# Kernel tuning notes

Hardware: AMD Instinct MI355X
Metric: run time of the kernel (lower is better)

## Reference

```python
import jax, jax.numpy as jnp
import numpy as np
import math

D_MODEL = 1024
NUM_HEADS = 16
SEQ = 2048
BATCH = 4


def setup_inputs() -> dict:
    key = jax.random.key(0)
    ks = jax.random.split(key, 7)
    s = 0.02
    return {
        "x": jax.random.normal(ks[0], (BATCH, SEQ, D_MODEL), jnp.float32),
        "Wq": jax.random.normal(ks[1], (D_MODEL, D_MODEL), jnp.float32) * s,
        "bq": jax.random.normal(ks[2], (D_MODEL,), jnp.float32) * s,
        "Wkv": jax.random.normal(ks[3], (D_MODEL, 2 * D_MODEL), jnp.float32) * s,
        "bkv": jax.random.normal(ks[4], (2 * D_MODEL,), jnp.float32) * s,
        "Wo": jax.random.normal(ks[5], (D_MODEL, D_MODEL), jnp.float32) * s,
        "bo": jax.random.normal(ks[6], (D_MODEL,), jnp.float32) * s,
        "decoderMask": 1,
    }


def reference(x, Wq, bq, Wkv, bkv, Wo, bo, decoderMask):
    B, S, D = x.shape
    H = NUM_HEADS
    dh = D // H
    q_ = x @ Wq + bq              # [B,S,D]
    kv_ = x @ Wkv + bkv           # [B,S,2D] (self-attention: m is None)
    # Faithful to source: concat [q_, kv_] then reshape into heads of 3*dh,
    # which interleaves Q/KV projection columns across heads.
    qkv = jnp.concatenate([q_, kv_], axis=-1)          # [B,S,3D]
    qkv = qkv.reshape(B, S, H, 3 * dh).transpose(0, 2, 1, 3)  # [B,H,S,3dh]
    q, k, v = jnp.split(qkv, 3, axis=-1)               # each [B,H,S,dh]
    scaled = jnp.einsum("bhqd,bhkd->bhqk", q, k) / math.sqrt(dh)
    if decoderMask:
        mask = jnp.triu(jnp.full((S, S), -jnp.inf, dtype=scaled.dtype), k=1)
        scaled = scaled + mask
    attn = jax.nn.softmax(scaled, axis=-1)
    vals = jnp.einsum("bhqk,bhkd->bhqd", attn, v)      # [B,H,S,dh]
    vals = vals.transpose(0, 2, 1, 3).reshape(B, S, D)
    return vals @ Wo + bo
```

## Files before the change

### kernel.cpp

```cpp
#include <hip/hip_runtime.h>
#include <cstddef>
#include <cstdint>

#define SEQ   2048
#define BATCH 4
#define DM    1024
#define NH    16
#define DH    64
#define ROWS  (BATCH*SEQ)
#define NC3   3072
#define SM_SCALE 0.18033688f

typedef unsigned short u16;
typedef __attribute__((ext_vector_type(8))) short bf16x8;
typedef __attribute__((ext_vector_type(2))) float f32x2;
typedef __attribute__((ext_vector_type(4))) float f32x4;
typedef __attribute__((ext_vector_type(16))) float f32x16;
typedef __attribute__((ext_vector_type(4))) unsigned u32x4;
typedef __attribute__((ext_vector_type(2))) unsigned u32x2;

union V16 { f32x16 v; f32x2 p[8]; };

__device__ __forceinline__ u16 f2b(float f) {
  union { float f; unsigned u; } v; v.f = f;
  unsigned r = v.u + 0x7fffu + ((v.u >> 16) & 1u);
  return (u16)(r >> 16);
}

__device__ __forceinline__ unsigned cvt_pk_bf16(float lo, float hi) {
  unsigned r;
  asm("v_cvt_pk_bf16_f32 %0, %1, %2" : "=v"(r) : "v"(lo), "v"(hi));
  return r;
}

__device__ __forceinline__ void plswap(unsigned& a, unsigned& b) {
  auto rr = __builtin_amdgcn_permlane32_swap((int)a, (int)b, false, false);
  a = (unsigned)rr[0];
  b = (unsigned)rr[1];
}

__device__ __forceinline__ float ex2(float x) { return __builtin_amdgcn_exp2f(x); }

__device__ __forceinline__ void gld16(const void* g, void* l) {
  __builtin_amdgcn_global_load_lds((const __attribute__((address_space(1))) void*)g,
                                   (__attribute__((address_space(3))) void*)l,
                                   16, 0, 0);
}

__global__ __launch_bounds__(256) void prep_tw_kernel(
    const float* __restrict__ x, const float* __restrict__ bq,
    const float* __restrict__ bkv, u16* __restrict__ xb, float* __restrict__ bc,
    const float* __restrict__ Wq, const float* __restrict__ Wkv,
    const float* __restrict__ Wo, u16* __restrict__ Wt)
{
  __shared__ float t_[32][33];
  const int tid = threadIdx.x;
  if (blockIdx.x < 8192) {
    int i = blockIdx.x * 256 + tid;
    int idx = i * 4;
    float4 v = *(const float4*)(x + idx);
    xb[idx + 0] = f2b(v.x);
    xb[idx + 1] = f2b(v.y);
    xb[idx + 2] = f2b(v.z);
    xb[idx + 3] = f2b(v.w);
    if (i < NC3) bc[i] = (i < DM) ? bq[i] : bkv[i - DM];
  } else {
    const int bid = blockIdx.x - 8192;
    const int n0 = (bid & 127) * 32, k0 = (bid >> 7) * 32;
    const int xcol = tid & 31, yrow = tid >> 5;
    #pragma unroll
    for (int it = 0; it < 4; ++it) {
      int k = k0 + yrow + it * 8;
      int n = n0 + xcol;
      float v;
      if (n < DM)           v = Wq[k * DM + n];
      else if (n < NC3)     v = Wkv[k * (2 * DM) + (n - DM)];
      else                  v = Wo[k * DM + (n - NC3)];
      t_[yrow + it * 8][xcol] = v;
    }
    __syncthreads();
    #pragma unroll
    for (int it = 0; it < 4; ++it) {
      int n = n0 + yrow + it * 8;
      int k = k0 + xcol;
      Wt[(size_t)n * DM + k] = f2b(t_[xcol][yrow + it * 8]);
    }
  }
}

template <int MODE>
__global__ __launch_bounds__(256) void gemm_bt(
    const u16* __restrict__ A, const u16* __restrict__ Bt,
    const float* __restrict__ bias, void* __restrict__ C,
    u16* __restrict__ Vt, int M, int N, int K)
{
  __shared__ alignas(16) u16 lds_[3 * 8192];
  const int tid = threadIdx.x;
  const int lane = tid & 63, wid = tid >> 6;
  const int wr = (wid >> 1) * 64, wc = (wid & 1) * 64;
  const int l15 = lane & 15, lhi = lane >> 4;

  const int bid = blockIdx.x;
  const int xcd = bid & 7, t = bid >> 3;
  const int rsub = t & 7, colb = t >> 3;
  const int row0 = (xcd * 8 + rsub) * 128, col0 = colb * 128;
  const int sr = tid >> 2;
  const int scol = (((tid & 3) ^ ((sr >> 1) & 3)) * 8);

  const u16* aS0 = A  + (size_t)(row0 + sr) * K + scol;
  const u16* aS1 = A  + (size_t)(row0 + 64 + sr) * K + scol;
  const u16* bS0 = Bt + (size_t)(col0 + sr) * K + scol;
  const u16* bS1 = Bt + (size_t)(col0 + 64 + sr) * K + scol;
  const int dA = tid * 8;

  const int csw = ((lhi ^ ((l15 >> 1) & 3)) * 8);
  int aoff[4], boff[4];
  #pragma unroll
  for (int m = 0; m < 4; ++m) aoff[m] = (wr + m * 16 + l15) * 32 + csw;
  #pragma unroll
  for (int n = 0; n < 4; ++n) boff[n] = 4096 + (wc + n * 16 + l15) * 32 + csw;

  f32x4 acc[4][4];
  #pragma unroll
  for (int m = 0; m < 4; ++m)
    #pragma unroll
    for (int n = 0; n < 4; ++n) { f32x4 z = {0.f, 0.f, 0.f, 0.f}; acc[m][n] = z; }

  const int KT = K >> 5;

  auto stage = [&](int kt, u16* base) {
    const int ka = kt * 32;
    gld16(aS0 + ka, base + dA);
    gld16(aS1 + ka, base + 2048 + dA);
    gld16(bS0 + ka, base + 4096 + dA);
    gld16(bS1 + ka, base + 6144 + dA);
  };

  u16* const bufA = lds_;
  u16* const bufB = lds_ + 8192;
  u16* const bufC = lds_ + 16384;

  stage(0, bufA); stage(1, bufB);
  asm volatile("s_waitcnt vmcnt(4)" ::: "memory");
  __builtin_amdgcn_s_barrier();

  u16* rb = bufA;
  u16* sb = bufC;
  for (int kt = 0; kt < KT; ++kt) {
    bf16x8 a[4], b[4];
    #pragma unroll
    for (int m = 0; m < 4; ++m) a[m] = *(const bf16x8*)&rb[aoff[m]];
    #pragma unroll
    for (int n = 0; n < 4; ++n) b[n] = *(const bf16x8*)&rb[boff[n]];
    if (kt + 2 < KT) stage(kt + 2, sb);
    __builtin_amdgcn_s_setprio(1);
    #pragma unroll
    for (int m = 0; m < 4; ++m)
      #pragma unroll
      for (int n = 0; n < 4; ++n)
        acc[m][n] = __builtin_amdgcn_mfma_f32_16x16x32_bf16(a[m], b[n], acc[m][n], 0, 0, 0);
    __builtin_amdgcn_s_setprio(0);
    if (kt + 1 < KT) {
      if (kt + 2 < KT) { asm volatile("s_waitcnt vmcnt(4)" ::: "memory"); }
      else             { asm volatile("s_waitcnt vmcnt(0)" ::: "memory"); }
      __builtin_amdgcn_s_barrier();
    }
    rb = (rb == bufC) ? bufA : rb + 8192;
    sb = (sb == bufC) ? bufA : sb + 8192;
  }

  #pragma unroll
  for (int m = 0; m < 4; ++m)
    #pragma unroll
    for (int n = 0; n < 4; ++n) {
      const int col = col0 + wc + n * 16 + l15;
      const float bv = bias[col];
      if (MODE == 0) {
        #pragma unroll
        for (int r = 0; r < 4; ++r) {
          const int row = row0 + wr + m * 16 + lhi * 4 + r;
          ((float*)C)[(size_t)row * N + col] = acc[m][n][r] + bv;
        }
      } else {
        const int hh = col / 192;
        const int cc = col - hh * 192;
        if (cc < 128) {
          const float qs = (cc < 64) ? SM_SCALE : 1.f;
          #pragma unroll
          for (int r = 0; r < 4; ++r) {
            const int row = row0 + wr + m * 16 + lhi * 4 + r;
            ((u16*)C)[(size_t)row * N + col] = f2b((acc[m][n][r] + bv) * qs);
          }
        } else {
          u16 wv[4];
          #pragma unroll
          for (int r = 0; r < 4; ++r) wv[r] = f2b(acc[m][n][r] + bv);
          const int row = row0 + wr + m * 16 + lhi * 4;
          const int bb = row >> 11, j = row & (SEQ - 1);
          u16* vt = Vt + ((size_t)(bb * NH + hh) * 64 + (cc - 128)) * SEQ + j;
          u32x2 pv = { (unsigned)wv[0] | ((unsigned)wv[1] << 16),
                       (unsigned)wv[2] | ((unsigned)wv[3] << 16) };
          *(u32x2*)vt = pv;
        }
      }
    }
}

__global__ __launch_bounds__(256) void attn_kernel(
    const u16* __restrict__ qkv, const u16* __restrict__ Vt, u16* __restrict__ ctx)
{
  const int bid = blockIdx.x;
  const int p   = (bid >> 3) & 7;
  const int g   = (bid & 7) + ((bid >> 6) << 3);
  const int h   = g & 15, b = g >> 4;
  const int tid = threadIdx.x;
  const int lane = tid & 63, wid = tid >> 6;
  const int l31 = lane & 31, lhi5 = lane >> 5;

  __shared__ alignas(16) u16 smem[4 * 64 * 64];

  const size_t kv_row = (size_t)(b * NH + h) * 64;
  const int sr = tid >> 3, sck = tid & 7;
  const int scks = sck ^ (sr & 7);

  const u16* kSrc0 = qkv + (size_t)(b * SEQ + sr) * NC3 + h * 192 + 64 + scks * 8;
  const u16* kSrc1 = kSrc0 + (size_t)32 * NC3;
  const u16* vSrc0 = Vt + (kv_row + sr) * SEQ + scks * 8;
  const u16* vSrc1 = vSrc0 + (size_t)32 * SEQ;
  const int dOff0 = sr * 64 + sck * 8;
  const int dOff1 = (32 + sr) * 64 + sck * 8;

  int koff[4], koff2[4];
  #pragma unroll
  for (int c = 0; c < 4; ++c) {
    koff[c]  = l31 * 64        + (((2 * c + lhi5) ^ (l31 & 7)) * 8);
    koff2[c] = (32 + l31) * 64 + (((2 * c + lhi5) ^ (l31 & 7)) * 8);
  }

  #pragma unroll 1
  for (int half = 0; half < 2; ++half) {
    const int qt = half ? (7 - p) : (8 + p);
    const int q0 = qt * 128;

    #pragma unroll
    for (int it = 0; it < 4; ++it) {
      int row = it * 32 + sr;
      gld16(qkv + (size_t)(b * SEQ + q0 + row) * NC3 + h * 192 + scks * 8,
            &smem[row * 64 + sck * 8]);
    }
    gld16(kSrc0, &smem[8192 + dOff0]);
    gld16(kSrc1, &smem[8192 + dOff1]);
    gld16(vSrc0, &smem[12288 + dOff0]);
    gld16(vSrc1, &smem[12288 + dOff1]);
    __syncthreads();

    bf16x8 qf[4];
    {
      const int qrow = wid * 32 + l31;
      #pragma unroll
      for (int c = 0; c < 4; ++c)
        qf[c] = *(const bf16x8*)&smem[qrow * 64 + (((2 * c + lhi5) ^ (qrow & 7)) * 8)];
    }
    __syncthreads();

    V16 o0, o1;
    #pragma unroll
    for (int r = 0; r < 16; ++r) { o0.v[r] = 0.f; o1.v[r] = 0.f; }
    float lrow = 0.f;

    const int nt = qt * 2 + 2;
    const int qw0 = q0 + wid * 32;
    const int qa  = qw0 + l31;
    const int dqb = qa - 4 * lhi5;

    for (int jt = 0; jt < nt; ++jt) {
      const int j0 = jt * 64;
      const u16* Kb = smem + ((jt & 1) ? 0 : 8192);
      const u16* Vb = smem + ((jt & 1) ? 4096 : 12288);

      if (jt + 1 < nt) {
        u16* Kn = smem + ((jt & 1) ? 8192 : 0);
        u16* Vn = smem + ((jt & 1) ? 12288 : 4096);
        const size_t kAdv = (size_t)(j0 + 64) * NC3;
        const int    vAdv = j0 + 64;
        gld16(kSrc0 + kAdv, &Kn[dOff0]);
        gld16(kSrc1 + kAdv, &Kn[dOff1]);
        gld16(vSrc0 + vAdv, &Vn[dOff0]);
        gld16(vSrc1 + vAdv, &Vn[dOff1]);
      }

      if (j0 <= qw0 + 31) {
        V16 s0, s1;
        #pragma unroll
        for (int r = 0; r < 16; ++r) { s0.v[r] = 0.f; s1.v[r] = 0.f; }
        __builtin_amdgcn_s_setprio(1);
        #pragma unroll
        for (int c = 0; c < 4; ++c) {
          bf16x8 kf = *(const bf16x8*)&Kb[koff[c]];
          s0.v = __builtin_amdgcn_mfma_f32_32x32x16_bf16(kf, qf[c], s0.v, 0, 0, 0);
        }
        #pragma unroll
        for (int c = 0; c < 4; ++c) {
          bf16x8 kf = *(const bf16x8*)&Kb[koff2[c]];
          s1.v = __builtin_amdgcn_mfma_f32_32x32x16_bf16(kf, qf[c], s1.v, 0, 0, 0);
        }
        __builtin_amdgcn_s_setprio(0);

        if (j0 + 63 > qw0) {
          const int dq = dqb - j0;
          #pragma unroll
          for (int r = 0; r < 16; ++r) {
            const int kvc = (r & 3) + 8 * (r >> 2);
            s0.v[r] = (kvc > dq)      ? -1e30f : s0.v[r];
            s1.v[r] = (kvc + 32 > dq) ? -1e30f : s1.v[r];
          }
        }

        f32x2 sum2 = {0.f, 0.f};
        #pragma unroll
        for (int i = 0; i < 8; ++i) {
          f32x2 e0, e1;
          e0[0] = ex2(s0.p[i][0]); e0[1] = ex2(s0.p[i][1]);
          e1[0] = ex2(s1.p[i][0]); e1[1] = ex2(s1.p[i][1]);
          s0.p[i] = e0; s1.p[i] = e1;
          sum2 += e0 + e1;
        }
        float ps = sum2[0] + sum2[1];
        {
          unsigned a = __builtin_bit_cast(unsigned, ps), bb = a;
          plswap(a, bb);
          ps = __builtin_bit_cast(float, a) + __builtin_bit_cast(float, bb);
        }
        lrow += ps;

        unsigned pk0[8], pk1[8];
        #pragma unroll
        for (int i = 0; i < 4; ++i) {
          pk0[2 * i]     = cvt_pk_bf16(s0.v[4 * i + 0], s0.v[4 * i + 1]);
          pk0[2 * i + 1] = cvt_pk_bf16(s0.v[4 * i + 2], s0.v[4 * i + 3]);
          pk1[2 * i]     = cvt_pk_bf16(s1.v[4 * i + 0], s1.v[4 * i + 1]);
          pk1[2 * i + 1] = cvt_pk_bf16(s1.v[4 * i + 2], s1.v[4 * i + 3]);
        }
        bf16x8 pf[4];
        {
          unsigned a0 = pk0[0], b0 = pk0[2]; plswap(a0, b0);
          unsigned a1 = pk0[1], b1 = pk0[3]; plswap(a1, b1);
          u32x4 w0v = {a0, a1, b0, b1}; pf[0] = __builtin_bit_cast(bf16x8, w0v);
          unsigned a2 = pk0[4], b2 = pk0[6]; plswap(a2, b2);
          unsigned a3 = pk0[5], b3 = pk0[7]; plswap(a3, b3);
          u32x4 w1v = {a2, a3, b2, b3}; pf[1] = __builtin_bit_cast(bf16x8, w1v);
          unsigned a4 = pk1[0], b4 = pk1[2]; plswap(a4, b4);
          unsigned a5 = pk1[1], b5 = pk1[3]; plswap(a5, b5);
          u32x4 w2v = {a4, a5, b4, b5}; pf[2] = __builtin_bit_cast(bf16x8, w2v);
          unsigned a6 = pk1[4], b6 = pk1[6]; plswap(a6, b6);
          unsigned a7 = pk1[5], b7 = pk1[7]; plswap(a7, b7);
          u32x4 w3v = {a6, a7, b6, b7}; pf[3] = __builtin_bit_cast(bf16x8, w3v);
        }

        __builtin_amdgcn_s_setprio(1);
        #pragma unroll
        for (int c = 0; c < 4; ++c) {
          bf16x8 vf = *(const bf16x8*)&Vb[koff[c]];
          o0.v = __builtin_amdgcn_mfma_f32_32x32x16_bf16(vf, pf[c], o0.v, 0, 0, 0);
        }
        #pragma unroll
        for (int c = 0; c < 4; ++c) {
          bf16x8 vf = *(const bf16x8*)&Vb[koff2[c]];
          o1.v = __builtin_amdgcn_mfma_f32_32x32x16_bf16(vf, pf[c], o1.v, 0, 0, 0);
        }
        __builtin_amdgcn_s_setprio(0);
      }
      __syncthreads();
    }

    const float inv = 1.f / lrow;
    u16* crow = ctx + (size_t)(b * SEQ + qa) * DM + h * DH;
    #pragma unroll
    for (int i = 0; i < 4; ++i) {
      u32x2 v0, v1;
      v0[0] = cvt_pk_bf16(o0.v[4 * i + 0] * inv, o0.v[4 * i + 1] * inv);
      v0[1] = cvt_pk_bf16(o0.v[4 * i + 2] * inv, o0.v[4 * i + 3] * inv);
      v1[0] = cvt_pk_bf16(o1.v[4 * i + 0] * inv, o1.v[4 * i + 1] * inv);
      v1[1] = cvt_pk_bf16(o1.v[4 * i + 2] * inv, o1.v[4 * i + 3] * inv);
      *(u32x2*)&crow[8 * i + 4 * lhi5]      = v0;
      *(u32x2*)&crow[32 + 8 * i + 4 * lhi5] = v1;
    }
  }
}

extern "C" void kernel_launch(void* const* d_in, const int* in_sizes, int n_in,
                              void* d_out, int out_size, void* d_ws, size_t ws_size,
                              hipStream_t stream) {
  (void)in_sizes; (void)n_in; (void)out_size; (void)ws_size;
  const float* x   = (const float*)d_in[0];
  const float* Wq  = (const float*)d_in[1];
  const float* bq  = (const float*)d_in[2];
  const float* Wkv = (const float*)d_in[3];
  const float* bkv = (const float*)d_in[4];
  const float* Wo  = (const float*)d_in[5];
  const float* bo  = (const float*)d_in[6];
  float* out = (float*)d_out;

  char* w = (char*)d_ws;
  size_t off = 0;
  auto alloc = [&](size_t bytes) { void* p = w + off; off += (bytes + 255) & ~(size_t)255; return p; };
  u16*   xb   = (u16*)alloc((size_t)ROWS * DM * 2);
  u16*   qkvb = (u16*)alloc((size_t)ROWS * NC3 * 2);
  u16*   Vt   = (u16*)alloc((size_t)BATCH * NH * DH * SEQ * 2);
  u16*   Wt   = (u16*)alloc((size_t)4096 * DM * 2);
  float* bc   = (float*)alloc((size_t)NC3 * 4);
  u16*   ctx  = xb;

  prep_tw_kernel<<<dim3(8192 + 4096), 256, 0, stream>>>(x, bq, bkv, xb, bc, Wq, Wkv, Wo, Wt);
  gemm_bt<1><<<dim3((ROWS / 128) * (NC3 / 128)), 256, 0, stream>>>(xb, Wt, bc, qkvb, Vt, ROWS, NC3, DM);
  attn_kernel<<<dim3(512), 256, 0, stream>>>(qkvb, Vt, ctx);
  gemm_bt<0><<<dim3((ROWS / 128) * (DM / 128)), 256, 0, stream>>>(ctx, Wt + (size_t)NC3 * DM, bo, out, nullptr, ROWS, DM, DM);
}
```

Measured before the change: 161.2 us.

## Replace QKV projection GEMM with 256x256-tile 8-wave pipelined kernel

Swaps the 128x128-tile, 4-wave QKV projection GEMM for a dedicated kernel that uses 256x256 tiles, 512 threads and 64-wide K steps. Global-to-LDS loads are interleaved across eight phases with barriers, and MFMA priority is raised. The larger tile increases operand reuse per LDS load and cuts global traffic. In exchange it uses 128 KB of LDS and many accumulator registers, and launches only 384 blocks, which risks occupancy and load balance across the CUs. The output GEMM is split into its own non-templated kernel with unchanged logic.

```diff
diff --git a/kernel.cpp b/kernel.cpp
--- a/kernel.cpp
+++ b/kernel.cpp
@@ -88,11 +88,151 @@
   }
 }
 
-template <int MODE>
-__global__ __launch_bounds__(256) void gemm_bt(
+__global__ __launch_bounds__(512, 2) void gemm8_qkv(
     const u16* __restrict__ A, const u16* __restrict__ Bt,
-    const float* __restrict__ bias, void* __restrict__ C,
-    u16* __restrict__ Vt, int M, int N, int K)
+    const float* __restrict__ bias, u16* __restrict__ C, u16* __restrict__ Vt)
+{
+  constexpr int K = 1024, N = NC3;
+  constexpr int ASLOT = 16384;
+  constexpr int HALF  = 8192;
+  constexpr int BBASE = 32768;
+  __shared__ alignas(16) u16 lds_[65536];
+
+  const int tid = threadIdx.x;
+  const int lane = tid & 63, wid = tid >> 6;
+  const int wr2 = wid >> 2, wc4 = wid & 3;
+  const int l15 = lane & 15, lhi = lane >> 4;
+
+  const int bid = blockIdx.x;
+  const int xcd = bid & 7, t = bid >> 3;
+  const int row0 = (xcd * 4 + (t & 3)) * 256;
+  const int col0 = (t >> 2) * 256;
+
+  const int sr = tid >> 3;
+  const int scg = ((tid & 7) ^ (sr & 7)) * 8;
+  const u16* aSrc = A  + (size_t)(row0 + sr) * K + scg;
+  const u16* bSrc = Bt + (size_t)(col0 + sr) * K + scg;
+  const int dLin = tid * 8;
+
+  auto stA = [&](int kt, int h) {
+    u16* d = lds_ + (kt & 1) * ASLOT + h * HALF + dLin;
+    const u16* s = aSrc + (size_t)(h * 128) * K + kt * 64;
+    gld16(s, d);
+    gld16(s + (size_t)64 * K, d + 4096);
+  };
+  auto stB = [&](int kt, int h) {
+    u16* d = lds_ + BBASE + (kt & 1) * ASLOT + h * HALF + dLin;
+    const u16* s = bSrc + (size_t)(h * 128) * K + kt * 64;
+    gld16(s, d);
+    gld16(s + (size_t)64 * K, d + 4096);
+  };
+
+  int csw[2];
+  csw[0] = ((lhi)     ^ (l15 & 7)) * 8;
+  csw[1] = ((4 + lhi) ^ (l15 & 7)) * 8;
+  const int aBase = wr2 * HALF + l15 * 64;
+  const int bBase = BBASE + (wc4 >> 1) * HALF + ((wc4 & 1) * 64 + l15) * 64;
+
+  f32x4 acc[8][4];
+  #pragma unroll
+  for (int m = 0; m < 8; ++m)
+    #pragma unroll
+    for (int n = 0; n < 4; ++n) { f32x4 z = {0.f, 0.f, 0.f, 0.f}; acc[m][n] = z; }
+
+  stA(0, 0); stA(0, 1); stB(0, 0); stB(0, 1); stB(1, 0); stB(1, 1);
+  asm volatile("s_waitcnt vmcnt(4)" ::: "memory");
+  __builtin_amdgcn_s_barrier();
+
+  constexpr int KT2 = K / 128;
+  for (int j = 0; j < KT2; ++j) {
+    const bool last = (j == KT2 - 1);
+    #pragma unroll
+    for (int hk = 0; hk < 2; ++hk) {
+      const int kt = 2 * j + hk;
+      const int slot = (kt & 1) * ASLOT;
+      bf16x8 bfr[4][2];
+      #pragma unroll
+      for (int ph = 0; ph < 4; ++ph) {
+        const int gp = hk * 4 + ph;
+        if (ph == 0) {
+          #pragma unroll
+          for (int n = 0; n < 4; ++n)
+            #pragma unroll
+            for (int kk = 0; kk < 2; ++kk)
+              bfr[n][kk] = *(const bf16x8*)&lds_[bBase + slot + n * 1024 + csw[kk]];
+        }
+        bf16x8 af[2][2];
+        #pragma unroll
+        for (int mi = 0; mi < 2; ++mi)
+          #pragma unroll
+          for (int kk = 0; kk < 2; ++kk)
+            af[mi][kk] = *(const bf16x8*)&lds_[aBase + slot + ph * 2048 + mi * 1024 + csw[kk]];
+        switch (gp) {
+          case 0: stA(2 * j + 1, 0); break;
+          case 1: stA(2 * j + 1, 1); break;
+          case 2: if (!last) stB(2 * j + 2, 0); break;
+          case 3: if (!last) stB(2 * j + 2, 1); break;
+          case 4: if (!last) stA(2 * j + 2, 0); break;
+          case 5: if (!last) stA(2 * j + 2, 1); break;
+          case 6: if (!last) stB(2 * j + 3, 0); break;
+          case 7: if (!last) stB(2 * j + 3, 1); break;
+        }
+        __builtin_amdgcn_s_barrier();
+        asm volatile("s_waitcnt lgkmcnt(0)" ::: "memory");
+        __builtin_amdgcn_sched_barrier(0);
+        __builtin_amdgcn_s_setprio(1);
+        #pragma unroll
+        for (int mi = 0; mi < 2; ++mi)
+          #pragma unroll
+          for (int n = 0; n < 4; ++n) {
+            acc[ph * 2 + mi][n] =
+                __builtin_amdgcn_mfma_f32_16x16x32_bf16(af[mi][0], bfr[n][0], acc[ph * 2 + mi][n], 0, 0, 0);
+            acc[ph * 2 + mi][n] =
+                __builtin_amdgcn_mfma_f32_16x16x32_bf16(af[mi][1], bfr[n][1], acc[ph * 2 + mi][n], 0, 0, 0);
+          }
+        __builtin_amdgcn_s_setprio(0);
+        if (gp == 3) {
+          if (last) { asm volatile("s_waitcnt vmcnt(0)" ::: "memory"); }
+          else      { asm volatile("s_waitcnt vmcnt(4)" ::: "memory"); }
+        } else if (gp == 7 && !last) {
+          asm volatile("s_waitcnt vmcnt(4)" ::: "memory");
+        }
+        __builtin_amdgcn_s_barrier();
+      }
+    }
+  }
+
+  #pragma unroll
+  for (int m = 0; m < 8; ++m) {
+    const int row = row0 + wr2 * 128 + m * 16 + lhi * 4;
+    #pragma unroll
+    for (int n = 0; n < 4; ++n) {
+      const int col = col0 + wc4 * 64 + n * 16 + l15;
+      const float bv = bias[col];
+      const int hh = col / 192;
+      const int cc = col - hh * 192;
+      if (cc < 128) {
+        const float qs = (cc < 64) ? SM_SCALE : 1.f;
+        #pragma unroll
+        for (int r = 0; r < 4; ++r)
+          C[(size_t)(row + r) * N + col] = f2b((acc[m][n][r] + bv) * qs);
+      } else {
+        u16 wv[4];
+        #pragma unroll
+        for (int r = 0; r < 4; ++r) wv[r] = f2b(acc[m][n][r] + bv);
+        const int bb = row >> 11, jj = row & (SEQ - 1);
+        u16* vt = Vt + ((size_t)(bb * NH + hh) * 64 + (cc - 128)) * SEQ + jj;
+        u32x2 pv = { (unsigned)wv[0] | ((unsigned)wv[1] << 16),
+                     (unsigned)wv[2] | ((unsigned)wv[3] << 16) };
+        *(u32x2*)vt = pv;
+      }
+    }
+  }
+}
+
+__global__ __launch_bounds__(256) void gemm_out(
+    const u16* __restrict__ A, const u16* __restrict__ Bt,
+    const float* __restrict__ bias, float* __restrict__ C, int M, int N, int K)
 {
   __shared__ alignas(16) u16 lds_[3 * 8192];
   const int tid = threadIdx.x;
@@ -127,7 +267,6 @@
     for (int n = 0; n < 4; ++n) { f32x4 z = {0.f, 0.f, 0.f, 0.f}; acc[m][n] = z; }
 
   const int KT = K >> 5;
-
   auto stage = [&](int kt, u16* base) {
     const int ka = kt * 32;
     gld16(aS0 + ka, base + dA);
@@ -175,33 +314,10 @@
     for (int n = 0; n < 4; ++n) {
       const int col = col0 + wc + n * 16 + l15;
       const float bv = bias[col];
-      if (MODE == 0) {
-        #pragma unroll
-        for (int r = 0; r < 4; ++r) {
-          const int row = row0 + wr + m * 16 + lhi * 4 + r;
-          ((float*)C)[(size_t)row * N + col] = acc[m][n][r] + bv;
-        }
-      } else {
-        const int hh = col / 192;
-        const int cc = col - hh * 192;
-        if (cc < 128) {
-          const float qs = (cc < 64) ? SM_SCALE : 1.f;
-          #pragma unroll
-          for (int r = 0; r < 4; ++r) {
-            const int row = row0 + wr + m * 16 + lhi * 4 + r;
-            ((u16*)C)[(size_t)row * N + col] = f2b((acc[m][n][r] + bv) * qs);
-          }
-        } else {
-          u16 wv[4];
-          #pragma unroll
-          for (int r = 0; r < 4; ++r) wv[r] = f2b(acc[m][n][r] + bv);
-          const int row = row0 + wr + m * 16 + lhi * 4;
-          const int bb = row >> 11, j = row & (SEQ - 1);
-          u16* vt = Vt + ((size_t)(bb * NH + hh) * 64 + (cc - 128)) * SEQ + j;
-          u32x2 pv = { (unsigned)wv[0] | ((unsigned)wv[1] << 16),
-                       (unsigned)wv[2] | ((unsigned)wv[3] << 16) };
-          *(u32x2*)vt = pv;
-        }
+      #pragma unroll
+      for (int r = 0; r < 4; ++r) {
+        const int row = row0 + wr + m * 16 + lhi * 4 + r;
+        C[(size_t)row * N + col] = acc[m][n][r] + bv;
       }
     }
 }
@@ -412,7 +528,7 @@
   u16*   ctx  = xb;
 
   prep_tw_kernel<<<dim3(8192 + 4096), 256, 0, stream>>>(x, bq, bkv, xb, bc, Wq, Wkv, Wo, Wt);
-  gemm_bt<1><<<dim3((ROWS / 128) * (NC3 / 128)), 256, 0, stream>>>(xb, Wt, bc, qkvb, Vt, ROWS, NC3, DM);
+  gemm8_qkv<<<dim3(384), 512, 0, stream>>>(xb, Wt, bc, qkvb, Vt);
   attn_kernel<<<dim3(512), 256, 0, stream>>>(qkvb, Vt, ctx);
-  gemm_bt<0><<<dim3((ROWS / 128) * (DM / 128)), 256, 0, stream>>>(ctx, Wt + (size_t)NC3 * DM, bo, out, nullptr, ROWS, DM, DM);
-}
+  gemm_out<<<dim3((ROWS / 128) * (DM / 128)), 256, 0, stream>>>(ctx, Wt + (size_t)NC3 * DM, bo, out, ROWS, DM, DM);
+}
```

Measured after the change: 161.6 us. About the same (+0.3%).
